# Performance work log

Hardware: AMD Instinct MI355X
Metric: run time of the kernel (lower is better)

The kernel has to match this reference:

```python
import jax, jax.numpy as jnp
import numpy as np

B, K, D, H = 4, 2048, 768, 12
HD = D // H
NEG = -1e30  # stands in for -inf in the additive mask


def setup_inputs() -> dict:
    key = jax.random.key(0)
    ks = jax.random.split(key, 11)
    s = 1.0 / np.sqrt(D)
    inp = {
        "x": jax.random.normal(ks[0], (B, K, D), jnp.float32),
        "is_context": jax.random.randint(ks[1], (B, K), 0, 2) > 0,
        "Wq": jax.random.normal(ks[2], (D, D), jnp.float32) * s,
        "bq": jax.random.normal(ks[3], (D,), jnp.float32) * 0.01,
        "Wk": jax.random.normal(ks[4], (D, D), jnp.float32) * s,
        "bk": jax.random.normal(ks[5], (D,), jnp.float32) * 0.01,
        "Wv": jax.random.normal(ks[6], (D, D), jnp.float32) * s,
        "bv": jax.random.normal(ks[7], (D,), jnp.float32) * 0.01,
        "Wo": jax.random.normal(ks[8], (D, D), jnp.float32) * s,
        "bo": jax.random.normal(ks[9], (D,), jnp.float32) * 0.01,
    }
    return inp


def reference(x, is_context, Wq, bq, Wk, bk, Wv, bv, Wo, bo):
    b, k_len, d = x.shape
    scale = 1.0 / jnp.sqrt(jnp.asarray(HD, x.dtype))
    # torch nn.Linear: y = x @ W.T + b
    q = (x @ Wq.T + bq).reshape(b, k_len, H, HD).transpose(0, 2, 1, 3)  # [B,H,K,hd]
    kk = (x @ Wk.T + bk).reshape(b, k_len, H, HD).transpose(0, 2, 1, 3)
    v = (x @ Wv.T + bv).reshape(b, k_len, H, HD).transpose(0, 2, 1, 3)

    ctx = is_context  # [B,K] bool
    # allowed[b,i,j]: context rows attend only to context cols; target rows attend to all
    allowed = (ctx[:, :, None] & ctx[:, None, :]) | (~ctx)[:, :, None]  # [B,K,K]

    scores = jnp.einsum("bhqd,bhkd->bhqk", q, kk) * scale  # [B,H,K,K]
    scores = jnp.where(allowed[:, None, :, :], scores, NEG)
    attn = jax.nn.softmax(scores, axis=-1)
    out = jnp.einsum("bhqk,bhkd->bhqd", attn, v)  # [B,H,K,hd]
    out = out.transpose(0, 2, 1, 3).reshape(b, k_len, d)
    return out @ Wo.T + bo
```

## Files before the change

### kernel.cpp

```cpp
#include <hip/hip_runtime.h>
#include <hip/hip_bf16.h>

constexpr int BATCH = 4;
constexpr int SEQ   = 2048;
constexpr int DIM   = 768;
constexpr int NH    = 12;
constexpr int HDIM  = 64;

typedef __attribute__((ext_vector_type(8))) short bf16x8;
typedef __attribute__((ext_vector_type(4))) float f32x4;
typedef __attribute__((ext_vector_type(4))) short s16x4;

__device__ inline short f2bf(float f) {
    union { float f; unsigned u; } v; v.f = f;
    unsigned r = (v.u + 0x7fff + ((v.u >> 16) & 1)) >> 16;
    return (short)r;
}

__device__ inline unsigned pack_bf16x2(float a, float b) {
    union { __hip_bfloat162 h; unsigned u; } c;
    c.h = __float22bfloat162_rn(make_float2(a, b));
    return c.u;
}

__device__ inline float fast_exp2(float x) {
#if __has_builtin(__builtin_amdgcn_exp2f)
    return __builtin_amdgcn_exp2f(x);
#else
    return __expf(x * 0.6931471805599453f);
#endif
}

__device__ inline float uint_as_float(unsigned u) {
    union { unsigned u; float f; } c; c.u = u; return c.f;
}

__device__ inline void gld16(const short* g, short* l) {
    __builtin_amdgcn_global_load_lds(
        (const __attribute__((address_space(1))) void*)g,
        (__attribute__((address_space(3))) void*)l, 16, 0, 0);
}

__global__ __launch_bounds__(256) void cast_bf16_kernel(
    const float* __restrict__ src, short* __restrict__ dst, int n4) {
    int i = blockIdx.x * blockDim.x + threadIdx.x;
    if (i >= n4) return;
    float4 v = ((const float4*)src)[i];
    s16x4 o;
    o.x = f2bf(v.x); o.y = f2bf(v.y); o.z = f2bf(v.z); o.w = f2bf(v.w);
    ((s16x4*)dst)[i] = o;
}

__global__ void detect_mask_kernel(const unsigned char* __restrict__ m,
                                   int nbytes, int* __restrict__ flag) {
    __shared__ int cnt;
    if (threadIdx.x == 0) cnt = 0;
    __syncthreads();
    int local = 0;
    for (int i = threadIdx.x; i < nbytes; i += blockDim.x) {
        if ((i & 3) != 0 && m[i] != 0) local++;
    }
    atomicAdd(&cnt, local);
    __syncthreads();
    if (threadIdx.x == 0) *flag = (cnt > 0) ? 1 : 0;
}

__device__ inline bool ctx_at(const void* p, bool isU8, int idx) {
    return isU8 ? (((const unsigned char*)p)[idx] != 0)
                : (((const int*)p)[idx] != 0);
}

template <bool BF16OUT>
__global__ __launch_bounds__(256) void gemm_mfma(
    const short* __restrict__ A,
    const short* __restrict__ W0, const float* __restrict__ bias0, void* __restrict__ C0,
    const short* __restrict__ W1, const float* __restrict__ bias1, void* __restrict__ C1,
    const short* __restrict__ W2, const float* __restrict__ bias2, void* __restrict__ C2,
    float scale0) {
    constexpr int N  = DIM;
    constexpr int Kd = DIM;

    const short* W; const float* bias; void* C; float scale;
    if (blockIdx.z == 0)      { W = W0; bias = bias0; C = C0; scale = scale0; }
    else if (blockIdx.z == 1) { W = W1; bias = bias1; C = C1; scale = 1.f; }
    else                      { W = W2; bias = bias2; C = C2; scale = 1.f; }

    const int tid  = threadIdx.x;
    const int wave = tid >> 6;
    const int lane = tid & 63;
    const int quad = lane >> 4;
    const int l16  = lane & 15;
    const int wm   = wave & 1;
    const int wn   = wave >> 1;
    const int m0   = blockIdx.y * 128;
    const int n0   = blockIdx.x * 128;

    __shared__ short As[128 * 32];
    __shared__ short Bs[128 * 32];

    const int srow = tid >> 2;
    const int skq  = tid & 3;
    const short* Ag = A + (size_t)(m0 + srow) * Kd + skq * 8;
    const short* Wg = W + (size_t)(n0 + srow) * Kd + skq * 8;
    short* AsP = As + srow * 32 + skq * 8;
    short* BsP = Bs + srow * 32 + skq * 8;

    f32x4 acc[4][4] = {};

    for (int kt = 0; kt < Kd; kt += 32) {
        __syncthreads();
        gld16(Ag + kt,                AsP);
        gld16(Ag + kt + 64 * Kd,      AsP + 64 * 32);
        gld16(Wg + kt,                BsP);
        gld16(Wg + kt + 64 * Kd,      BsP + 64 * 32);
        __syncthreads();

        bf16x8 af[4], bfr[4];
#pragma unroll
        for (int mt = 0; mt < 4; ++mt)
            af[mt] = *(const bf16x8*)&As[(wm * 64 + mt * 16 + l16) * 32 + quad * 8];
#pragma unroll
        for (int nt = 0; nt < 4; ++nt)
            bfr[nt] = *(const bf16x8*)&Bs[(wn * 64 + nt * 16 + l16) * 32 + quad * 8];
#pragma unroll
        for (int mt = 0; mt < 4; ++mt)
#pragma unroll
            for (int nt = 0; nt < 4; ++nt)
                acc[mt][nt] = __builtin_amdgcn_mfma_f32_16x16x32_bf16(
                    af[mt], bfr[nt], acc[mt][nt], 0, 0, 0);
    }

    float bv[4];
#pragma unroll
    for (int nt = 0; nt < 4; ++nt) bv[nt] = bias[n0 + wn * 64 + nt * 16 + l16];

#pragma unroll
    for (int mt = 0; mt < 4; ++mt)
#pragma unroll
        for (int nt = 0; nt < 4; ++nt)
#pragma unroll
            for (int reg = 0; reg < 4; ++reg) {
                const int m = m0 + wm * 64 + mt * 16 + quad * 4 + reg;
                const int n = n0 + wn * 64 + nt * 16 + l16;
                const float v = (acc[mt][nt][reg] + bv[nt]) * scale;
                if (BF16OUT) ((short*)C)[(size_t)m * N + n] = f2bf(v);
                else         ((float*)C)[(size_t)m * N + n] = v;
            }
}

__global__ __launch_bounds__(256) void attn_mfma2(
    const short* __restrict__ Qb, const short* __restrict__ Kb,
    const short* __restrict__ Vb, const void* __restrict__ ctxp,
    const int* __restrict__ flagp, short* __restrict__ Ob) {
    const int b    = blockIdx.z;
    const int h    = blockIdx.y;
    const int q0   = blockIdx.x * 128;
    const int tid  = threadIdx.x;
    const int wave = tid >> 6;
    const int lane = tid & 63;
    const int quad = lane >> 4;
    const int l16  = lane & 15;
    const bool isU8 = (*flagp != 0);

    __shared__ short Ks[64][72];
    __shared__ short Vt[64][72];
    __shared__ short Ps[4][32][72];

    bf16x8 qf[2][2];
#pragma unroll
    for (int rg = 0; rg < 2; ++rg) {
        const short* qp = Qb + (size_t)(b * SEQ + q0 + wave * 32 + rg * 16 + l16) * DIM
                        + h * HDIM + quad * 8;
        qf[rg][0] = *(const bf16x8*)qp;
        qf[rg][1] = *(const bf16x8*)(qp + 32);
    }

    unsigned mbits[2][4];
#pragma unroll
    for (int rg = 0; rg < 2; ++rg)
#pragma unroll
        for (int reg = 0; reg < 4; ++reg)
            mbits[rg][reg] = ctx_at(ctxp, isU8,
                b * SEQ + q0 + wave * 32 + rg * 16 + quad * 4 + reg) ? 0xFFFFFFFFu : 0u;

    const unsigned negu = [] { union { float f; unsigned u; } c; c.f = -1e30f; return c.u; }();

    float l_r[2][4] = {};
    f32x4 acc[2][4] = {};

    for (int t = 0; t < SEQ / 64; ++t) {
        const int k0 = t * 64;
        __syncthreads();
        {
            const int key = tid >> 2, d0 = (tid & 3) * 16;
            const uint4* src = (const uint4*)(Kb + (size_t)(b * SEQ + k0 + key) * DIM
                                              + h * HDIM + d0);
            *(uint4*)&Ks[key][d0]     = src[0];
            *(uint4*)&Ks[key][d0 + 8] = src[1];
        }
        {
            const int kl = tid & 15;
            const int d0 = (tid >> 4) * 4;
            s16x4 vr[4];
#pragma unroll
            for (int g = 0; g < 4; ++g)
                vr[g] = *(const s16x4*)(Vb + (size_t)(b * SEQ + k0 + g * 16 + kl) * DIM
                                        + h * HDIM + d0);
#pragma unroll
            for (int i = 0; i < 4; ++i) {
                s16x4 w = {vr[0][i], vr[1][i], vr[2][i], vr[3][i]};
                *(s16x4*)&Vt[d0 + i][4 * kl] = w;
            }
        }
        __syncthreads();

        const unsigned long long kmask =
            __ballot(ctx_at(ctxp, isU8, b * SEQ + k0 + lane));
        unsigned kaddb[4];
#pragma unroll
        for (int g = 0; g < 4; ++g)
            kaddb[g] = ((kmask >> (g * 16 + l16)) & 1ull) ? 0u : negu;

        f32x4 s4[2][4] = {};
#pragma unroll
        for (int ks = 0; ks < 2; ++ks) {
            bf16x8 kf[4];
#pragma unroll
            for (int g = 0; g < 4; ++g)
                kf[g] = *(const bf16x8*)&Ks[g * 16 + l16][ks * 32 + quad * 8];
#pragma unroll
            for (int g = 0; g < 4; ++g) {
                s4[0][g] = __builtin_amdgcn_mfma_f32_16x16x32_bf16(qf[0][ks], kf[g], s4[0][g], 0, 0, 0);
                s4[1][g] = __builtin_amdgcn_mfma_f32_16x16x32_bf16(qf[1][ks], kf[g], s4[1][g], 0, 0, 0);
            }
        }

#pragma unroll
        for (int rg = 0; rg < 2; ++rg)
#pragma unroll
            for (int reg = 0; reg < 4; ++reg) {
                const int row = rg * 16 + quad * 4 + reg;
                float p[4];
#pragma unroll
                for (int g = 0; g < 4; ++g)
                    p[g] = fast_exp2(s4[rg][g][reg]
                                     + uint_as_float(mbits[rg][reg] & kaddb[g]));
                l_r[rg][reg] += (p[0] + p[1]) + (p[2] + p[3]);
                uint2 w;
                w.x = pack_bf16x2(p[0], p[1]);
                w.y = pack_bf16x2(p[2], p[3]);
                *(uint2*)&Ps[wave][row][4 * l16] = w;
            }

#pragma unroll
        for (int ks = 0; ks < 2; ++ks) {
            bf16x8 pf0 = *(const bf16x8*)&Ps[wave][l16][ks * 32 + quad * 8];
            bf16x8 pf1 = *(const bf16x8*)&Ps[wave][16 + l16][ks * 32 + quad * 8];
#pragma unroll
            for (int dt = 0; dt < 4; ++dt) {
                bf16x8 vf = *(const bf16x8*)&Vt[dt * 16 + l16][ks * 32 + quad * 8];
                acc[0][dt] = __builtin_amdgcn_mfma_f32_16x16x32_bf16(pf0, vf, acc[0][dt], 0, 0, 0);
                acc[1][dt] = __builtin_amdgcn_mfma_f32_16x16x32_bf16(pf1, vf, acc[1][dt], 0, 0, 0);
            }
        }
    }

    float inv[2][4];
#pragma unroll
    for (int rg = 0; rg < 2; ++rg)
#pragma unroll
        for (int reg = 0; reg < 4; ++reg) {
            float l = l_r[rg][reg];
            l += __shfl_xor(l, 1);
            l += __shfl_xor(l, 2);
            l += __shfl_xor(l, 4);
            l += __shfl_xor(l, 8);
            inv[rg][reg] = 1.f / l;
        }

#pragma unroll
    for (int rg = 0; rg < 2; ++rg)
#pragma unroll
        for (int dt = 0; dt < 4; ++dt)
#pragma unroll
            for (int reg = 0; reg < 4; ++reg) {
                const int q = q0 + wave * 32 + rg * 16 + quad * 4 + reg;
                Ob[(size_t)(b * SEQ + q) * DIM + h * HDIM + dt * 16 + l16] =
                    f2bf(acc[rg][dt][reg] * inv[rg][reg]);
            }
}

extern "C" void kernel_launch(void* const* d_in, const int* in_sizes, int n_in,
                              void* d_out, int out_size, void* d_ws, size_t ws_size,
                              hipStream_t stream) {
    const float* x   = (const float*)d_in[0];
    const void*  ctx = d_in[1];
    const float* Wq  = (const float*)d_in[2];
    const float* bq  = (const float*)d_in[3];
    const float* Wk  = (const float*)d_in[4];
    const float* bk  = (const float*)d_in[5];
    const float* Wv  = (const float*)d_in[6];
    const float* bv  = (const float*)d_in[7];
    const float* Wo  = (const float*)d_in[8];
    const float* bo  = (const float*)d_in[9];
    float* out = (float*)d_out;

    char* ws = (char*)d_ws;
    int* flag = (int*)ws;
    const size_t bufbf = (size_t)BATCH * SEQ * DIM * sizeof(short);
    const size_t wbuf  = (size_t)DIM * DIM * sizeof(short);
    short* xb  = (short*)(ws + 256);
    short* Qb  = (short*)(ws + 256 + bufbf);
    short* Kb  = (short*)(ws + 256 + 2 * bufbf);
    short* Vb  = (short*)(ws + 256 + 3 * bufbf);
    short* Ab  = (short*)(ws + 256 + 4 * bufbf);
    short* Wqb = (short*)(ws + 256 + 5 * bufbf);
    short* Wkb = (short*)(ws + 256 + 5 * bufbf + wbuf);
    short* Wvb = (short*)(ws + 256 + 5 * bufbf + 2 * wbuf);
    short* Wob = (short*)(ws + 256 + 5 * bufbf + 3 * wbuf);

    detect_mask_kernel<<<1, 256, 0, stream>>>((const unsigned char*)ctx,
                                              BATCH * SEQ, flag);

    const int nx4 = BATCH * SEQ * DIM / 4;
    const int nw4 = DIM * DIM / 4;
    cast_bf16_kernel<<<(nx4 + 255) / 256, 256, 0, stream>>>(x, xb, nx4);
    cast_bf16_kernel<<<(nw4 + 255) / 256, 256, 0, stream>>>(Wq, Wqb, nw4);
    cast_bf16_kernel<<<(nw4 + 255) / 256, 256, 0, stream>>>(Wk, Wkb, nw4);
    cast_bf16_kernel<<<(nw4 + 255) / 256, 256, 0, stream>>>(Wv, Wvb, nw4);
    cast_bf16_kernel<<<(nw4 + 255) / 256, 256, 0, stream>>>(Wo, Wob, nw4);

    dim3 gQKV(DIM / 128, (BATCH * SEQ) / 128, 3);
    gemm_mfma<true><<<gQKV, 256, 0, stream>>>(
        xb, Wqb, bq, Qb, Wkb, bk, Kb, Wvb, bv, Vb, 0.125f * 1.4426950408889634f);

    dim3 gAttn(SEQ / 128, NH, BATCH);
    attn_mfma2<<<gAttn, 256, 0, stream>>>(Qb, Kb, Vb, ctx, flag, Ab);

    dim3 gOut(DIM / 128, (BATCH * SEQ) / 128, 1);
    gemm_mfma<false><<<gOut, 256, 0, stream>>>(
        Ab, Wob, bo, out, Wob, bo, out, Wob, bo, out, 1.f);
}
```

Baseline: 297.8 us.

## Halve attention query tile, mask via bit-AND, row sums via MFMA, fuse prep kernels

The attention kernel now gives each wave 16 query rows instead of 32, so the grid doubles and fewer registers are live, and launch bounds request 5 blocks per CU. Masking no longer adds -1e30 before exp; it zeroes the packed bf16 probabilities with bitwise AND masks. Row sums are computed by an MFMA against a ones vector, which replaces the scalar accumulation and the shuffle reduction. The five cast kernels and the mask-detect kernel are merged into one launch. The cost is that each K/V tile loaded into LDS is reused by half as many query rows, and the row sums now come from bf16-rounded probabilities.

```diff
diff --git a/kernel.cpp b/kernel.cpp
--- a/kernel.cpp
+++ b/kernel.cpp
@@ -31,43 +31,57 @@
 #endif
 }
 
-__device__ inline float uint_as_float(unsigned u) {
-    union { unsigned u; float f; } c; c.u = u; return c.f;
-}
-
 __device__ inline void gld16(const short* g, short* l) {
     __builtin_amdgcn_global_load_lds(
         (const __attribute__((address_space(1))) void*)g,
         (__attribute__((address_space(3))) void*)l, 16, 0, 0);
 }
 
-__global__ __launch_bounds__(256) void cast_bf16_kernel(
-    const float* __restrict__ src, short* __restrict__ dst, int n4) {
-    int i = blockIdx.x * blockDim.x + threadIdx.x;
-    if (i >= n4) return;
+__device__ inline bool ctx_at(const void* p, bool isU8, int idx) {
+    return isU8 ? (((const unsigned char*)p)[idx] != 0)
+                : (((const int*)p)[idx] != 0);
+}
+
+__global__ __launch_bounds__(256) void prep_kernel(
+    const float* __restrict__ x,  const float* __restrict__ Wq,
+    const float* __restrict__ Wk, const float* __restrict__ Wv,
+    const float* __restrict__ Wo,
+    short* __restrict__ xb,  short* __restrict__ Wqb,
+    short* __restrict__ Wkb, short* __restrict__ Wvb,
+    short* __restrict__ Wob,
+    const unsigned char* __restrict__ ctxm, int ctxbytes, int* __restrict__ flag) {
+    const int blk = blockIdx.x;
+    constexpr int XBLK = (BATCH * SEQ * DIM / 4) / 256;
+    constexpr int WBLK = (DIM * DIM / 4) / 256;
+
+    if (blk == XBLK + 4 * WBLK) {
+        __shared__ int cnt;
+        if (threadIdx.x == 0) cnt = 0;
+        __syncthreads();
+        int local = 0;
+        for (int i = threadIdx.x; i < ctxbytes; i += 256)
+            if ((i & 3) != 0 && ctxm[i] != 0) local++;
+        atomicAdd(&cnt, local);
+        __syncthreads();
+        if (threadIdx.x == 0) *flag = (cnt > 0) ? 1 : 0;
+        return;
+    }
+
+    const float* src; short* dst; int i;
+    if (blk < XBLK) {
+        src = x; dst = xb;
+        i = blk * 256 + threadIdx.x;
+    } else {
+        const int r = blk - XBLK;
+        const int w = r / WBLK;
+        src = (w == 0) ? Wq : (w == 1) ? Wk : (w == 2) ? Wv : Wo;
+        dst = (w == 0) ? Wqb : (w == 1) ? Wkb : (w == 2) ? Wvb : Wob;
+        i = (r - w * WBLK) * 256 + threadIdx.x;
+    }
     float4 v = ((const float4*)src)[i];
     s16x4 o;
     o.x = f2bf(v.x); o.y = f2bf(v.y); o.z = f2bf(v.z); o.w = f2bf(v.w);
     ((s16x4*)dst)[i] = o;
-}
-
-__global__ void detect_mask_kernel(const unsigned char* __restrict__ m,
-                                   int nbytes, int* __restrict__ flag) {
-    __shared__ int cnt;
-    if (threadIdx.x == 0) cnt = 0;
-    __syncthreads();
-    int local = 0;
-    for (int i = threadIdx.x; i < nbytes; i += blockDim.x) {
-        if ((i & 3) != 0 && m[i] != 0) local++;
-    }
-    atomicAdd(&cnt, local);
-    __syncthreads();
-    if (threadIdx.x == 0) *flag = (cnt > 0) ? 1 : 0;
-}
-
-__device__ inline bool ctx_at(const void* p, bool isU8, int idx) {
-    return isU8 ? (((const unsigned char*)p)[idx] != 0)
-                : (((const int*)p)[idx] != 0);
 }
 
 template <bool BF16OUT>
@@ -148,13 +162,13 @@
             }
 }
 
-__global__ __launch_bounds__(256) void attn_mfma2(
+__global__ __launch_bounds__(256, 5) void attn_mfma3(
     const short* __restrict__ Qb, const short* __restrict__ Kb,
     const short* __restrict__ Vb, const void* __restrict__ ctxp,
     const int* __restrict__ flagp, short* __restrict__ Ob) {
     const int b    = blockIdx.z;
     const int h    = blockIdx.y;
-    const int q0   = blockIdx.x * 128;
+    const int q0   = blockIdx.x * 64;
     const int tid  = threadIdx.x;
     const int wave = tid >> 6;
     const int lane = tid & 63;
@@ -164,29 +178,28 @@
 
     __shared__ short Ks[64][72];
     __shared__ short Vt[64][72];
-    __shared__ short Ps[4][32][72];
-
-    bf16x8 qf[2][2];
-#pragma unroll
-    for (int rg = 0; rg < 2; ++rg) {
-        const short* qp = Qb + (size_t)(b * SEQ + q0 + wave * 32 + rg * 16 + l16) * DIM
+    __shared__ short Ps[4][16][72];
+
+    bf16x8 qf[2];
+    {
+        const short* qp = Qb + (size_t)(b * SEQ + q0 + wave * 16 + l16) * DIM
                         + h * HDIM + quad * 8;
-        qf[rg][0] = *(const bf16x8*)qp;
-        qf[rg][1] = *(const bf16x8*)(qp + 32);
-    }
-
-    unsigned mbits[2][4];
-#pragma unroll
-    for (int rg = 0; rg < 2; ++rg)
-#pragma unroll
-        for (int reg = 0; reg < 4; ++reg)
-            mbits[rg][reg] = ctx_at(ctxp, isU8,
-                b * SEQ + q0 + wave * 32 + rg * 16 + quad * 4 + reg) ? 0xFFFFFFFFu : 0u;
-
-    const unsigned negu = [] { union { float f; unsigned u; } c; c.f = -1e30f; return c.u; }();
-
-    float l_r[2][4] = {};
-    f32x4 acc[2][4] = {};
+        qf[0] = *(const bf16x8*)qp;
+        qf[1] = *(const bf16x8*)(qp + 32);
+    }
+
+    unsigned nmb[4];
+#pragma unroll
+    for (int reg = 0; reg < 4; ++reg)
+        nmb[reg] = ctx_at(ctxp, isU8, b * SEQ + q0 + wave * 16 + quad * 4 + reg)
+                   ? 0u : 0xFFFFFFFFu;
+
+    bf16x8 ones;
+#pragma unroll
+    for (int i = 0; i < 8; ++i) ones[i] = (short)0x3F80;
+
+    f32x4 accl = {};
+    f32x4 acc[4] = {};
 
     for (int t = 0; t < SEQ / 64; ++t) {
         const int k0 = t * 64;
@@ -216,12 +229,15 @@
 
         const unsigned long long kmask =
             __ballot(ctx_at(ctxp, isU8, b * SEQ + k0 + lane));
-        unsigned kaddb[4];
-#pragma unroll
-        for (int g = 0; g < 4; ++g)
-            kaddb[g] = ((kmask >> (g * 16 + l16)) & 1ull) ? 0u : negu;
-
-        f32x4 s4[2][4] = {};
+        unsigned km2[2];
+#pragma unroll
+        for (int gp = 0; gp < 2; ++gp) {
+            const unsigned lo = (unsigned)((kmask >> (gp * 32 + l16)) & 1ull);
+            const unsigned hi = (unsigned)((kmask >> (gp * 32 + 16 + l16)) & 1ull);
+            km2[gp] = (lo ? 0x0000FFFFu : 0u) | (hi ? 0xFFFF0000u : 0u);
+        }
+
+        f32x4 s4[4] = {};
 #pragma unroll
         for (int ks = 0; ks < 2; ++ks) {
             bf16x8 kf[4];
@@ -229,65 +245,45 @@
             for (int g = 0; g < 4; ++g)
                 kf[g] = *(const bf16x8*)&Ks[g * 16 + l16][ks * 32 + quad * 8];
 #pragma unroll
-            for (int g = 0; g < 4; ++g) {
-                s4[0][g] = __builtin_amdgcn_mfma_f32_16x16x32_bf16(qf[0][ks], kf[g], s4[0][g], 0, 0, 0);
-                s4[1][g] = __builtin_amdgcn_mfma_f32_16x16x32_bf16(qf[1][ks], kf[g], s4[1][g], 0, 0, 0);
-            }
-        }
-
-#pragma unroll
-        for (int rg = 0; rg < 2; ++rg)
-#pragma unroll
-            for (int reg = 0; reg < 4; ++reg) {
-                const int row = rg * 16 + quad * 4 + reg;
-                float p[4];
-#pragma unroll
-                for (int g = 0; g < 4; ++g)
-                    p[g] = fast_exp2(s4[rg][g][reg]
-                                     + uint_as_float(mbits[rg][reg] & kaddb[g]));
-                l_r[rg][reg] += (p[0] + p[1]) + (p[2] + p[3]);
-                uint2 w;
-                w.x = pack_bf16x2(p[0], p[1]);
-                w.y = pack_bf16x2(p[2], p[3]);
-                *(uint2*)&Ps[wave][row][4 * l16] = w;
-            }
+            for (int g = 0; g < 4; ++g)
+                s4[g] = __builtin_amdgcn_mfma_f32_16x16x32_bf16(qf[ks], kf[g], s4[g], 0, 0, 0);
+        }
+
+#pragma unroll
+        for (int reg = 0; reg < 4; ++reg) {
+            const float p0 = fast_exp2(s4[0][reg]);
+            const float p1 = fast_exp2(s4[1][reg]);
+            const float p2 = fast_exp2(s4[2][reg]);
+            const float p3 = fast_exp2(s4[3][reg]);
+            uint2 w;
+            w.x = pack_bf16x2(p0, p1) & (nmb[reg] | km2[0]);
+            w.y = pack_bf16x2(p2, p3) & (nmb[reg] | km2[1]);
+            *(uint2*)&Ps[wave][quad * 4 + reg][4 * l16] = w;
+        }
 
 #pragma unroll
         for (int ks = 0; ks < 2; ++ks) {
-            bf16x8 pf0 = *(const bf16x8*)&Ps[wave][l16][ks * 32 + quad * 8];
-            bf16x8 pf1 = *(const bf16x8*)&Ps[wave][16 + l16][ks * 32 + quad * 8];
+            bf16x8 pf = *(const bf16x8*)&Ps[wave][l16][ks * 32 + quad * 8];
+            accl = __builtin_amdgcn_mfma_f32_16x16x32_bf16(pf, ones, accl, 0, 0, 0);
 #pragma unroll
             for (int dt = 0; dt < 4; ++dt) {
                 bf16x8 vf = *(const bf16x8*)&Vt[dt * 16 + l16][ks * 32 + quad * 8];
-                acc[0][dt] = __builtin_amdgcn_mfma_f32_16x16x32_bf16(pf0, vf, acc[0][dt], 0, 0, 0);
-                acc[1][dt] = __builtin_amdgcn_mfma_f32_16x16x32_bf16(pf1, vf, acc[1][dt], 0, 0, 0);
+                acc[dt] = __builtin_amdgcn_mfma_f32_16x16x32_bf16(pf, vf, acc[dt], 0, 0, 0);
             }
         }
     }
 
-    float inv[2][4];
-#pragma unroll
-    for (int rg = 0; rg < 2; ++rg)
+    float inv[4];
+#pragma unroll
+    for (int reg = 0; reg < 4; ++reg) inv[reg] = 1.f / accl[reg];
+#pragma unroll
+    for (int dt = 0; dt < 4; ++dt)
 #pragma unroll
         for (int reg = 0; reg < 4; ++reg) {
-            float l = l_r[rg][reg];
-            l += __shfl_xor(l, 1);
-            l += __shfl_xor(l, 2);
-            l += __shfl_xor(l, 4);
-            l += __shfl_xor(l, 8);
-            inv[rg][reg] = 1.f / l;
-        }
-
-#pragma unroll
-    for (int rg = 0; rg < 2; ++rg)
-#pragma unroll
-        for (int dt = 0; dt < 4; ++dt)
-#pragma unroll
-            for (int reg = 0; reg < 4; ++reg) {
-                const int q = q0 + wave * 32 + rg * 16 + quad * 4 + reg;
-                Ob[(size_t)(b * SEQ + q) * DIM + h * HDIM + dt * 16 + l16] =
-                    f2bf(acc[rg][dt][reg] * inv[rg][reg]);
-            }
+            const int q = q0 + wave * 16 + quad * 4 + reg;
+            Ob[(size_t)(b * SEQ + q) * DIM + h * HDIM + dt * 16 + l16] =
+                f2bf(acc[dt][reg] * inv[reg]);
+        }
 }
 
 extern "C" void kernel_launch(void* const* d_in, const int* in_sizes, int n_in,
@@ -319,23 +315,18 @@
     short* Wvb = (short*)(ws + 256 + 5 * bufbf + 2 * wbuf);
     short* Wob = (short*)(ws + 256 + 5 * bufbf + 3 * wbuf);
 
-    detect_mask_kernel<<<1, 256, 0, stream>>>((const unsigned char*)ctx,
-                                              BATCH * SEQ, flag);
-
-    const int nx4 = BATCH * SEQ * DIM / 4;
-    const int nw4 = DIM * DIM / 4;
-    cast_bf16_kernel<<<(nx4 + 255) / 256, 256, 0, stream>>>(x, xb, nx4);
-    cast_bf16_kernel<<<(nw4 + 255) / 256, 256, 0, stream>>>(Wq, Wqb, nw4);
-    cast_bf16_kernel<<<(nw4 + 255) / 256, 256, 0, stream>>>(Wk, Wkb, nw4);
-    cast_bf16_kernel<<<(nw4 + 255) / 256, 256, 0, stream>>>(Wv, Wvb, nw4);
-    cast_bf16_kernel<<<(nw4 + 255) / 256, 256, 0, stream>>>(Wo, Wob, nw4);
+    constexpr int XBLK = (BATCH * SEQ * DIM / 4) / 256;
+    constexpr int WBLK = (DIM * DIM / 4) / 256;
+    prep_kernel<<<XBLK + 4 * WBLK + 1, 256, 0, stream>>>(
+        x, Wq, Wk, Wv, Wo, xb, Wqb, Wkb, Wvb, Wob,
+        (const unsigned char*)ctx, BATCH * SEQ, flag);
 
     dim3 gQKV(DIM / 128, (BATCH * SEQ) / 128, 3);
     gemm_mfma<true><<<gQKV, 256, 0, stream>>>(
         xb, Wqb, bq, Qb, Wkb, bk, Kb, Wvb, bv, Vb, 0.125f * 1.4426950408889634f);
 
-    dim3 gAttn(SEQ / 128, NH, BATCH);
-    attn_mfma2<<<gAttn, 256, 0, stream>>>(Qb, Kb, Vb, ctx, flag, Ab);
+    dim3 gAttn(SEQ / 64, NH, BATCH);
+    attn_mfma3<<<gAttn, 256, 0, stream>>>(Qb, Kb, Vb, ctx, flag, Ab);
 
     dim3 gOut(DIM / 128, (BATCH * SEQ) / 128, 1);
     gemm_mfma<false><<<gOut, 256, 0, stream>>>(
```

After: 321.7 us. 1.08x slower.
